# Kernel optimization log

Hardware: AMD Instinct MI355X
Metric: run time of the kernel (lower is better)

The kernel has to match this reference:

```python
import jax, jax.numpy as jnp
import numpy as np

N = 200_000   # nodes in batched graph
E = 400_000   # edges
D = 128       # embed_dim
L = 5         # num_layer
G = 1000      # number of graphs in batch
ATOM_V = 119  # atom vocab (OGB)
BOND_V = 5    # bond vocab (OGB)
OUT = 128     # output_dim
EPS = 1e-5


def setup_inputs() -> dict:
    key = jax.random.key(0)
    ks = jax.random.split(key, 16)
    inp = {
        "nfeat": jax.random.randint(ks[0], (N,), 0, ATOM_V),
        "efeat": jax.random.randint(ks[1], (E,), 0, BOND_V),
        "src": jax.random.randint(ks[2], (E,), 0, N),
        "dst": jax.random.randint(ks[3], (E,), 0, N),
        "node2graph": jnp.sort(jax.random.randint(ks[4], (N,), 0, G)),
        # learned parameters
        "atom_emb": jax.random.normal(ks[5], (ATOM_V, D), jnp.float32) * 0.02,
        "edge_emb": jax.random.normal(ks[6], (L, BOND_V, D), jnp.float32) * 0.02,
        "W": jax.random.normal(ks[7], (L, D, D), jnp.float32) * 0.02,
        "b": jnp.zeros((L, D), jnp.float32),
        "gamma": jnp.ones((L, D), jnp.float32),
        "beta": jnp.zeros((L, D), jnp.float32),
        "W1": jax.random.normal(ks[8], (D, D), jnp.float32) * 0.02,
        "b1": jnp.zeros((D,), jnp.float32),
        "W2": jax.random.normal(ks[9], (D, OUT), jnp.float32) * 0.02,
        "b2": jnp.zeros((OUT,), jnp.float32),
    }
    return inp


def reference(nfeat, efeat, src, dst, node2graph,
              atom_emb, edge_emb, W, b, gamma, beta, W1, b1, W2, b2):
    h = atom_emb[nfeat]                                  # [N, D]
    # in-degree + 1 (GCNConvLayer degree norm)
    deg = jax.ops.segment_sum(jnp.ones((E,), h.dtype), dst, num_segments=N) + 1.0
    for l in range(L):
        e = edge_emb[l][efeat]                           # [E, D] edge encoder
        m = h[src] + e                                   # u_add_e
        neigh = jax.ops.segment_sum(m, dst, num_segments=N)  # fn.sum -> 'neigh'
        h = ((h + neigh) / deg[:, None]) @ W[l] + b[l]   # project_node_feat
        # batch norm over nodes (training-mode batch stats), affine
        mu = jnp.mean(h, axis=0)
        var = jnp.var(h, axis=0)
        h = (h - mu) * jax.lax.rsqrt(var + EPS) * gamma[l] + beta[l]
        h = jax.nn.relu(h)                               # activation; dropout=eval
    # global mean pooling per graph
    cnt = jax.ops.segment_sum(jnp.ones((N,), h.dtype), node2graph, num_segments=G)
    g = jax.ops.segment_sum(h, node2graph, num_segments=G) / jnp.maximum(cnt, 1.0)[:, None]
    # predict MLP (dropout in eval mode = identity)
    out = jax.nn.relu(g @ W1 + b1) @ W2 + b2             # [G, OUT]
    return out
```

## Files before the change

kernel.cpp:

```cpp
#include <hip/hip_runtime.h>
#include <hip/hip_bf16.h>
#include <cstddef>

#define NN 200000
#define NE 400000
#define DD 128
#define NL 5
#define NG 1000
#define BOND_V 5
#define BM 32
#define NBLK (NN / BM)
#define MAXD 16
#define CHUNK 200
#define NB_SCAN 200
#define CH 1000
#define SB 125
#define EPS 1e-5f
#define XS 136

typedef __bf16 bf16x8 __attribute__((ext_vector_type(8)));
typedef float floatx4 __attribute__((ext_vector_type(4)));

__device__ __forceinline__ unsigned short f2bf(float f) {
    unsigned int u = __float_as_uint(f);
    u = (u + 0x7fffu + ((u >> 16) & 1u)) >> 16;
    return (unsigned short)u;
}
__device__ __forceinline__ float bf2f(unsigned short s) {
    return __uint_as_float(((unsigned int)s) << 16);
}
__device__ __forceinline__ float4 bf4_to_f4(uint2 v) {
    float4 o;
    o.x = __uint_as_float(v.x << 16);
    o.y = __uint_as_float(v.x & 0xffff0000u);
    o.z = __uint_as_float(v.y << 16);
    o.w = __uint_as_float(v.y & 0xffff0000u);
    return o;
}
__device__ __forceinline__ float4 actv4(float4 h, float4 sc, float4 sh) {
    float4 o;
    o.x = fmaxf(0.f, h.x * sc.x + sh.x);
    o.y = fmaxf(0.f, h.y * sc.y + sh.y);
    o.z = fmaxf(0.f, h.z * sc.z + sh.z);
    o.w = fmaxf(0.f, h.w * sc.w + sh.w);
    return o;
}

__global__ void k_setup1(const int* __restrict__ dst, int* __restrict__ cnt,
                         const int* __restrict__ n2g, float* __restrict__ gcnt,
                         const float* __restrict__ W, unsigned short* __restrict__ Wht,
                         unsigned short* __restrict__ Wlt) {
    int e = blockIdx.x * blockDim.x + threadIdx.x;
    if (e < NE) atomicAdd(&cnt[dst[e]], 1);
    if (e < NN) atomicAdd(&gcnt[n2g[e]], 1.0f);
    if (e < NL * DD * DD) {
        int l = e / (DD * DD), rem = e % (DD * DD);
        int k = rem / DD, n = rem % DD;
        float v = W[e];
        unsigned short hb = f2bf(v);
        unsigned short lb = f2bf(v - bf2f(hb));
        size_t o = (size_t)l * DD * DD + (size_t)n * DD + k;
        Wht[o] = hb; Wlt[o] = lb;
    }
}

__global__ void k_scan1(const int* __restrict__ cnt, int* __restrict__ bsum) {
    __shared__ int sh[256];
    int b = blockIdx.x, t = threadIdx.x;
    int s = 0;
    if (t < CH / 4) {
        int base = b * CH + t * 4;
        s = cnt[base] + cnt[base + 1] + cnt[base + 2] + cnt[base + 3];
    }
    sh[t] = s;
    __syncthreads();
    if (t == 0) {
        int tot = 0;
        for (int i = 0; i < CH / 4; i++) tot += sh[i];
        bsum[b] = tot;
    }
}

__global__ void k_scan2(const int* __restrict__ bsum, int* __restrict__ bpre,
                        int* __restrict__ off) {
    if (threadIdx.x == 0) {
        int run = 0;
        for (int i = 0; i < NB_SCAN; i++) { bpre[i] = run; run += bsum[i]; }
        off[NN] = NE;
    }
}

__global__ void k_scan3(const int* __restrict__ cnt, const int* __restrict__ bpre,
                        int* __restrict__ off, int* __restrict__ cur,
                        float* __restrict__ rdeg) {
    __shared__ int sh[256];
    int b = blockIdx.x, t = threadIdx.x;
    int base = b * CH + t * 4;
    int c0 = 0, c1 = 0, c2 = 0, c3 = 0, s = 0;
    if (t < CH / 4) {
        c0 = cnt[base]; c1 = cnt[base + 1]; c2 = cnt[base + 2]; c3 = cnt[base + 3];
        s = c0 + c1 + c2 + c3;
    }
    sh[t] = s;
    __syncthreads();
    if (t == 0) {
        int run = bpre[b];
        for (int i = 0; i < CH / 4; i++) { int v = sh[i]; sh[i] = run; run += v; }
    }
    __syncthreads();
    if (t < CH / 4) {
        int run = sh[t];
        off[base] = run; cur[base] = run; run += c0;
        off[base + 1] = run; cur[base + 1] = run; run += c1;
        off[base + 2] = run; cur[base + 2] = run; run += c2;
        off[base + 3] = run; cur[base + 3] = run;
        rdeg[base]     = 1.0f / (float)(c0 + 1);
        rdeg[base + 1] = 1.0f / (float)(c1 + 1);
        rdeg[base + 2] = 1.0f / (float)(c2 + 1);
        rdeg[base + 3] = 1.0f / (float)(c3 + 1);
    }
}

__global__ void k_bucket(const int* __restrict__ src, const int* __restrict__ dst,
                         const int* __restrict__ efeat, int* __restrict__ cur,
                         int* __restrict__ esrc, int* __restrict__ eft) {
    int e = blockIdx.x * blockDim.x + threadIdx.x;
    if (e < NE) {
        int p = atomicAdd(&cur[dst[e]], 1);
        esrc[p] = src[e];
        eft[p] = efeat[e];
    }
}

__global__ void k_pad(const int* __restrict__ off, const int* __restrict__ esrc,
                      const int* __restrict__ eft, const int* __restrict__ nfeat,
                      int* __restrict__ pent, int* __restrict__ pent0,
                      int* __restrict__ bperm, int* __restrict__ gmax) {
    __shared__ int offL[BM + 1];
    __shared__ int degS[BM];
    __shared__ int sortIdx[BM];
    __shared__ int gmaxS[8];
    int b = blockIdx.x, tid = threadIdx.x;
    if (tid <= BM) offL[tid] = off[b * BM + tid];
    __syncthreads();
    if (tid < BM) degS[tid] = offL[tid + 1] - offL[tid];
    __syncthreads();
    if (tid < BM) {
        int d = degS[tid], rank = 0;
        #pragma unroll
        for (int j = 0; j < BM; j++)
            rank += (degS[j] > d) || (degS[j] == d && j < tid);
        sortIdx[rank] = tid;
    }
    __syncthreads();
    if (tid < 8) {
        int g = degS[sortIdx[tid * 4]];
        gmaxS[tid] = g;
        gmax[b * 8 + tid] = g;
    }
    if (tid < BM) bperm[b * BM + tid] = sortIdx[tid];
    __syncthreads();
    for (int idx = tid; idx < BM * MAXD; idx += 256) {
        int p = idx & 31, j = idx >> 5, g = p >> 2;
        int gm = gmaxS[g]; if (gm > MAXD) gm = MAXD;
        if (j < gm) {
            int row = sortIdx[p];
            int d = degS[row];
            int v, v0;
            if (j < d) {
                int e = offL[row] + j;
                int s = esrc[e], f = eft[e];
                v = s | (f << 18);
                v0 = nfeat[s] | (f << 18);
            } else { v = (5 << 18); v0 = (5 << 18); }
            pent[(size_t)b * MAXD * BM + j * BM + p] = v;
            pent0[(size_t)b * MAXD * BM + j * BM + p] = v0;
        }
    }
}

__global__ __launch_bounds__(256, 4)
void k_fused(const void* __restrict__ basep, const int* __restrict__ nfeat, int first,
             const int* __restrict__ off, const int* __restrict__ esrc,
             const int* __restrict__ eft, const int* __restrict__ pentsel,
             const int* __restrict__ bperm, const int* __restrict__ gmax,
             const float* __restrict__ eemb, const float* __restrict__ rdeg,
             const float* __restrict__ scP, const float* __restrict__ shP,
             const unsigned short* __restrict__ Wht, const unsigned short* __restrict__ Wlt,
             const float* __restrict__ bias,
             unsigned short* __restrict__ C, float* __restrict__ part) {
    __shared__ unsigned short Xh[BM * XS];
    __shared__ unsigned short Xl[BM * XS];
    __shared__ float eSr[6 * DD];
    __shared__ int pentL[BM * MAXD];
    __shared__ int offL[BM + 1];
    __shared__ int permL[BM];
    __shared__ int gmL[8];

    const float* baseF = (const float*)basep;
    const unsigned short* baseB = (const unsigned short*)basep;

    int tid = threadIdx.x;
    int n0 = blockIdx.x * BM;
    if (tid < 160) *(float4*)(eSr + tid * 4) = *(const float4*)(eemb + tid * 4);
    else if (tid < 192) *(float4*)(eSr + tid * 4) = (float4){0.f, 0.f, 0.f, 0.f};
    if (tid <= BM) offL[tid] = off[n0 + tid];
    if (tid < BM) permL[tid] = bperm[blockIdx.x * BM + tid];
    if (tid < 8) gmL[tid] = gmax[blockIdx.x * 8 + tid];
    {
        const int2* pg = (const int2*)(pentsel + (size_t)blockIdx.x * MAXD * BM);
        *(int2*)(pentL + tid * 2) = pg[tid];
    }

    int lane32 = tid & 31, grp = tid >> 5;
    int c4 = lane32 << 2;
    float4 sc4, sh4;
    if (!first) {
        sc4 = *(const float4*)(scP + c4);
        sh4 = *(const float4*)(shP + c4);
    }
    __syncthreads();

    int rows[4];
    #pragma unroll
    for (int i = 0; i < 4; i++) rows[i] = permL[grp * 4 + i];

    float4 acc[4];
    #pragma unroll
    for (int i = 0; i < 4; i++) {
        int n = n0 + rows[i];
        if (first) {
            acc[i] = *(const float4*)(baseF + (size_t)nfeat[n] * DD + c4);
        } else {
            uint2 g = *(const uint2*)(baseB + (size_t)n * DD + c4);
            acc[i] = actv4(bf4_to_f4(g), sc4, sh4);
        }
    }

    int gmx = gmL[grp];
    int jmax = gmx < MAXD ? gmx : MAXD;
    const int* pL = pentL + grp * 4;
    int j = 0;
    if (first) {
        for (; j + 2 <= jmax; j += 2) {
            int a0 = pL[j*32+0], a1 = pL[j*32+1], a2 = pL[j*32+2], a3 = pL[j*32+3];
            int b0 = pL[j*32+32], b1 = pL[j*32+33], b2 = pL[j*32+34], b3 = pL[j*32+35];
            float4 ha0 = *(const float4*)(baseF + (size_t)(a0 & 0x3FFFF) * DD + c4);
            float4 ha1 = *(const float4*)(baseF + (size_t)(a1 & 0x3FFFF) * DD + c4);
            float4 ha2 = *(const float4*)(baseF + (size_t)(a2 & 0x3FFFF) * DD + c4);
            float4 ha3 = *(const float4*)(baseF + (size_t)(a3 & 0x3FFFF) * DD + c4);
            float4 hb0 = *(const float4*)(baseF + (size_t)(b0 & 0x3FFFF) * DD + c4);
            float4 hb1 = *(const float4*)(baseF + (size_t)(b1 & 0x3FFFF) * DD + c4);
            float4 hb2 = *(const float4*)(baseF + (size_t)(b2 & 0x3FFFF) * DD + c4);
            float4 hb3 = *(const float4*)(baseF + (size_t)(b3 & 0x3FFFF) * DD + c4);
            int fa0 = a0 >> 18, fa1 = a1 >> 18, fa2 = a2 >> 18, fa3 = a3 >> 18;
            int fb0 = b0 >> 18, fb1 = b1 >> 18, fb2 = b2 >> 18, fb3 = b3 >> 18;
            float wa0 = (fa0 == 5) ? 0.f : 1.f, wa1 = (fa1 == 5) ? 0.f : 1.f;
            float wa2 = (fa2 == 5) ? 0.f : 1.f, wa3 = (fa3 == 5) ? 0.f : 1.f;
            float wb0 = (fb0 == 5) ? 0.f : 1.f, wb1 = (fb1 == 5) ? 0.f : 1.f;
            float wb2 = (fb2 == 5) ? 0.f : 1.f, wb3 = (fb3 == 5) ? 0.f : 1.f;
            float4 ea0 = *(const float4*)(eSr + fa0 * DD + c4);
            float4 ea1 = *(const float4*)(eSr + fa1 * DD + c4);
            float4 ea2 = *(const float4*)(eSr + fa2 * DD + c4);
            float4 ea3 = *(const float4*)(eSr + fa3 * DD + c4);
            float4 eb0 = *(const float4*)(eSr + fb0 * DD + c4);
            float4 eb1 = *(const float4*)(eSr + fb1 * DD + c4);
            float4 eb2 = *(const float4*)(eSr + fb2 * DD + c4);
            float4 eb3 = *(const float4*)(eSr + fb3 * DD + c4);
            acc[0].x += (ha0.x + ea0.x) * wa0 + (hb0.x + eb0.x) * wb0;
            acc[0].y += (ha0.y + ea0.y) * wa0 + (hb0.y + eb0.y) * wb0;
            acc[0].z += (ha0.z + ea0.z) * wa0 + (hb0.z + eb0.z) * wb0;
            acc[0].w += (ha0.w + ea0.w) * wa0 + (hb0.w + eb0.w) * wb0;
            acc[1].x += (ha1.x + ea1.x) * wa1 + (hb1.x + eb1.x) * wb1;
            acc[1].y += (ha1.y + ea1.y) * wa1 + (hb1.y + eb1.y) * wb1;
            acc[1].z += (ha1.z + ea1.z) * wa1 + (hb1.z + eb1.z) * wb1;
            acc[1].w += (ha1.w + ea1.w) * wa1 + (hb1.w + eb1.w) * wb1;
            acc[2].x += (ha2.x + ea2.x) * wa2 + (hb2.x + eb2.x) * wb2;
            acc[2].y += (ha2.y + ea2.y) * wa2 + (hb2.y + eb2.y) * wb2;
            acc[2].z += (ha2.z + ea2.z) * wa2 + (hb2.z + eb2.z) * wb2;
            acc[2].w += (ha2.w + ea2.w) * wa2 + (hb2.w + eb2.w) * wb2;
            acc[3].x += (ha3.x + ea3.x) * wa3 + (hb3.x + eb3.x) * wb3;
            acc[3].y += (ha3.y + ea3.y) * wa3 + (hb3.y + eb3.y) * wb3;
            acc[3].z += (ha3.z + ea3.z) * wa3 + (hb3.z + eb3.z) * wb3;
            acc[3].w += (ha3.w + ea3.w) * wa3 + (hb3.w + eb3.w) * wb3;
        }
        for (; j < jmax; j++) {
            int a0 = pL[j*32+0], a1 = pL[j*32+1], a2 = pL[j*32+2], a3 = pL[j*32+3];
            float4 h0 = *(const float4*)(baseF + (size_t)(a0 & 0x3FFFF) * DD + c4);
            float4 h1 = *(const float4*)(baseF + (size_t)(a1 & 0x3FFFF) * DD + c4);
            float4 h2 = *(const float4*)(baseF + (size_t)(a2 & 0x3FFFF) * DD + c4);
            float4 h3 = *(const float4*)(baseF + (size_t)(a3 & 0x3FFFF) * DD + c4);
            int f0 = a0 >> 18, f1 = a1 >> 18, f2 = a2 >> 18, f3 = a3 >> 18;
            float w0 = (f0 == 5) ? 0.f : 1.f, w1 = (f1 == 5) ? 0.f : 1.f;
            float w2 = (f2 == 5) ? 0.f : 1.f, w3 = (f3 == 5) ? 0.f : 1.f;
            float4 e0 = *(const float4*)(eSr + f0 * DD + c4);
            float4 e1 = *(const float4*)(eSr + f1 * DD + c4);
            float4 e2 = *(const float4*)(eSr + f2 * DD + c4);
            float4 e3 = *(const float4*)(eSr + f3 * DD + c4);
            acc[0].x += (h0.x + e0.x) * w0; acc[0].y += (h0.y + e0.y) * w0;
            acc[0].z += (h0.z + e0.z) * w0; acc[0].w += (h0.w + e0.w) * w0;
            acc[1].x += (h1.x + e1.x) * w1; acc[1].y += (h1.y + e1.y) * w1;
            acc[1].z += (h1.z + e1.z) * w1; acc[1].w += (h1.w + e1.w) * w1;
            acc[2].x += (h2.x + e2.x) * w2; acc[2].y += (h2.y + e2.y) * w2;
            acc[2].z += (h2.z + e2.z) * w2; acc[2].w += (h2.w + e2.w) * w2;
            acc[3].x += (h3.x + e3.x) * w3; acc[3].y += (h3.y + e3.y) * w3;
            acc[3].z += (h3.z + e3.z) * w3; acc[3].w += (h3.w + e3.w) * w3;
        }
    } else {
        for (; j + 2 <= jmax; j += 2) {
            int a0 = pL[j*32+0], a1 = pL[j*32+1], a2 = pL[j*32+2], a3 = pL[j*32+3];
            int b0 = pL[j*32+32], b1 = pL[j*32+33], b2 = pL[j*32+34], b3 = pL[j*32+35];
            uint2 ga0 = *(const uint2*)(baseB + (size_t)(a0 & 0x3FFFF) * DD + c4);
            uint2 ga1 = *(const uint2*)(baseB + (size_t)(a1 & 0x3FFFF) * DD + c4);
            uint2 ga2 = *(const uint2*)(baseB + (size_t)(a2 & 0x3FFFF) * DD + c4);
            uint2 ga3 = *(const uint2*)(baseB + (size_t)(a3 & 0x3FFFF) * DD + c4);
            uint2 gb0 = *(const uint2*)(baseB + (size_t)(b0 & 0x3FFFF) * DD + c4);
            uint2 gb1 = *(const uint2*)(baseB + (size_t)(b1 & 0x3FFFF) * DD + c4);
            uint2 gb2 = *(const uint2*)(baseB + (size_t)(b2 & 0x3FFFF) * DD + c4);
            uint2 gb3 = *(const uint2*)(baseB + (size_t)(b3 & 0x3FFFF) * DD + c4);
            float4 ha0 = actv4(bf4_to_f4(ga0), sc4, sh4);
            float4 ha1 = actv4(bf4_to_f4(ga1), sc4, sh4);
            float4 ha2 = actv4(bf4_to_f4(ga2), sc4, sh4);
            float4 ha3 = actv4(bf4_to_f4(ga3), sc4, sh4);
            float4 hb0 = actv4(bf4_to_f4(gb0), sc4, sh4);
            float4 hb1 = actv4(bf4_to_f4(gb1), sc4, sh4);
            float4 hb2 = actv4(bf4_to_f4(gb2), sc4, sh4);
            float4 hb3 = actv4(bf4_to_f4(gb3), sc4, sh4);
            int fa0 = a0 >> 18, fa1 = a1 >> 18, fa2 = a2 >> 18, fa3 = a3 >> 18;
            int fb0 = b0 >> 18, fb1 = b1 >> 18, fb2 = b2 >> 18, fb3 = b3 >> 18;
            float wa0 = (fa0 == 5) ? 0.f : 1.f, wa1 = (fa1 == 5) ? 0.f : 1.f;
            float wa2 = (fa2 == 5) ? 0.f : 1.f, wa3 = (fa3 == 5) ? 0.f : 1.f;
            float wb0 = (fb0 == 5) ? 0.f : 1.f, wb1 = (fb1 == 5) ? 0.f : 1.f;
            float wb2 = (fb2 == 5) ? 0.f : 1.f, wb3 = (fb3 == 5) ? 0.f : 1.f;
            float4 ea0 = *(const float4*)(eSr + fa0 * DD + c4);
            float4 ea1 = *(const float4*)(eSr + fa1 * DD + c4);
            float4 ea2 = *(const float4*)(eSr + fa2 * DD + c4);
            float4 ea3 = *(const float4*)(eSr + fa3 * DD + c4);
            float4 eb0 = *(const float4*)(eSr + fb0 * DD + c4);
            float4 eb1 = *(const float4*)(eSr + fb1 * DD + c4);
            float4 eb2 = *(const float4*)(eSr + fb2 * DD + c4);
            float4 eb3 = *(const float4*)(eSr + fb3 * DD + c4);
            acc[0].x += (ha0.x + ea0.x) * wa0 + (hb0.x + eb0.x) * wb0;
            acc[0].y += (ha0.y + ea0.y) * wa0 + (hb0.y + eb0.y) * wb0;
            acc[0].z += (ha0.z + ea0.z) * wa0 + (hb0.z + eb0.z) * wb0;
            acc[0].w += (ha0.w + ea0.w) * wa0 + (hb0.w + eb0.w) * wb0;
            acc[1].x += (ha1.x + ea1.x) * wa1 + (hb1.x + eb1.x) * wb1;
            acc[1].y += (ha1.y + ea1.y) * wa1 + (hb1.y + eb1.y) * wb1;
            acc[1].z += (ha1.z + ea1.z) * wa1 + (hb1.z + eb1.z) * wb1;
            acc[1].w += (ha1.w + ea1.w) * wa1 + (hb1.w + eb1.w) * wb1;
            acc[2].x += (ha2.x + ea2.x) * wa2 + (hb2.x + eb2.x) * wb2;
            acc[2].y += (ha2.y + ea2.y) * wa2 + (hb2.y + eb2.y) * wb2;
            acc[2].z += (ha2.z + ea2.z) * wa2 + (hb2.z + eb2.z) * wb2;
            acc[2].w += (ha2.w + ea2.w) * wa2 + (hb2.w + eb2.w) * wb2;
            acc[3].x += (ha3.x + ea3.x) * wa3 + (hb3.x + eb3.x) * wb3;
            acc[3].y += (ha3.y + ea3.y) * wa3 + (hb3.y + eb3.y) * wb3;
            acc[3].z += (ha3.z + ea3.z) * wa3 + (hb3.z + eb3.z) * wb3;
            acc[3].w += (ha3.w + ea3.w) * wa3 + (hb3.w + eb3.w) * wb3;
        }
        for (; j < jmax; j++) {
            int a0 = pL[j*32+0], a1 = pL[j*32+1], a2 = pL[j*32+2], a3 = pL[j*32+3];
            uint2 g0 = *(const uint2*)(baseB + (size_t)(a0 & 0x3FFFF) * DD + c4);
            uint2 g1 = *(const uint2*)(baseB + (size_t)(a1 & 0x3FFFF) * DD + c4);
            uint2 g2 = *(const uint2*)(baseB + (size_t)(a2 & 0x3FFFF) * DD + c4);
            uint2 g3 = *(const uint2*)(baseB + (size_t)(a3 & 0x3FFFF) * DD + c4);
            float4 h0 = actv4(bf4_to_f4(g0), sc4, sh4);
            float4 h1 = actv4(bf4_to_f4(g1), sc4, sh4);
            float4 h2 = actv4(bf4_to_f4(g2), sc4, sh4);
            float4 h3 = actv4(bf4_to_f4(g3), sc4, sh4);
            int f0 = a0 >> 18, f1 = a1 >> 18, f2 = a2 >> 18, f3 = a3 >> 18;
            float w0 = (f0 == 5) ? 0.f : 1.f, w1 = (f1 == 5) ? 0.f : 1.f;
            float w2 = (f2 == 5) ? 0.f : 1.f, w3 = (f3 == 5) ? 0.f : 1.f;
            float4 e0 = *(const float4*)(eSr + f0 * DD + c4);
            float4 e1 = *(const float4*)(eSr + f1 * DD + c4);
            float4 e2 = *(const float4*)(eSr + f2 * DD + c4);
            float4 e3 = *(const float4*)(eSr + f3 * DD + c4);
            acc[0].x += (h0.x + e0.x) * w0; acc[0].y += (h0.y + e0.y) * w0;
            acc[0].z += (h0.z + e0.z) * w0; acc[0].w += (h0.w + e0.w) * w0;
            acc[1].x += (h1.x + e1.x) * w1; acc[1].y += (h1.y + e1.y) * w1;
            acc[1].z += (h1.z + e1.z) * w1; acc[1].w += (h1.w + e1.w) * w1;
            acc[2].x += (h2.x + e2.x) * w2; acc[2].y += (h2.y + e2.y) * w2;
            acc[2].z += (h2.z + e2.z) * w2; acc[2].w += (h2.w + e2.w) * w2;
            acc[3].x += (h3.x + e3.x) * w3; acc[3].y += (h3.y + e3.y) * w3;
            acc[3].z += (h3.z + e3.z) * w3; acc[3].w += (h3.w + e3.w) * w3;
        }
    }

    if (gmx > MAXD) {
        #pragma unroll
        for (int i = 0; i < 4; i++) {
            int row = rows[i];
            for (int e = offL[row] + MAXD; e < offL[row + 1]; e++) {
                int s = esrc[e], f = eft[e];
                float4 hv;
                if (first) {
                    hv = *(const float4*)(baseF + (size_t)nfeat[s] * DD + c4);
                } else {
                    uint2 g = *(const uint2*)(baseB + (size_t)s * DD + c4);
                    hv = actv4(bf4_to_f4(g), sc4, sh4);
                }
                const float* ep = eSr + f * DD + c4;
                acc[i].x += hv.x + ep[0]; acc[i].y += hv.y + ep[1];
                acc[i].z += hv.z + ep[2]; acc[i].w += hv.w + ep[3];
            }
        }
    }

    #pragma unroll
    for (int i = 0; i < 4; i++) {
        int r = rows[i];
        float rd = rdeg[n0 + r];
        float ax = acc[i].x * rd, ay = acc[i].y * rd, az = acc[i].z * rd, aw = acc[i].w * rd;
        unsigned short h0 = f2bf(ax), h1 = f2bf(ay), h2 = f2bf(az), h3 = f2bf(aw);
        unsigned short l0 = f2bf(ax - bf2f(h0));
        unsigned short l1 = f2bf(ay - bf2f(h1));
        unsigned short l2 = f2bf(az - bf2f(h2));
        unsigned short l3 = f2bf(aw - bf2f(h3));
        uint2 hv2, lv2;
        hv2.x = (unsigned)h0 | ((unsigned)h1 << 16);
        hv2.y = (unsigned)h2 | ((unsigned)h3 << 16);
        lv2.x = (unsigned)l0 | ((unsigned)l1 << 16);
        lv2.y = (unsigned)l2 | ((unsigned)l3 << 16);
        *(uint2*)(Xh + r * XS + c4) = hv2;
        *(uint2*)(Xl + r * XS + c4) = lv2;
    }
    __syncthreads();

    int lane = tid & 63, w = tid >> 6;
    int m16 = lane & 15, quad = lane >> 4;
    int rowTile = w & 1;
    int colBase = (w >> 1) << 6;
    int rowA = rowTile * 16 + m16;

    floatx4 acc4[4];
    #pragma unroll
    for (int t = 0; t < 4; t++) acc4[t] = (floatx4){0.f, 0.f, 0.f, 0.f};

    #pragma unroll
    for (int kp = 0; kp < 4; kp++) {
        bf16x8 ah = *(const bf16x8*)(Xh + rowA * XS + kp * 32 + quad * 8);
        bf16x8 al = *(const bf16x8*)(Xl + rowA * XS + kp * 32 + quad * 8);
        #pragma unroll
        for (int t = 0; t < 4; t++) {
            int ncol = colBase + t * 16 + m16;
            bf16x8 bh = *(const bf16x8*)(Wht + (size_t)ncol * DD + kp * 32 + quad * 8);
            bf16x8 bl = *(const bf16x8*)(Wlt + (size_t)ncol * DD + kp * 32 + quad * 8);
            acc4[t] = __builtin_amdgcn_mfma_f32_16x16x32_bf16(ah, bh, acc4[t], 0, 0, 0);
            acc4[t] = __builtin_amdgcn_mfma_f32_16x16x32_bf16(ah, bl, acc4[t], 0, 0, 0);
            acc4[t] = __builtin_amdgcn_mfma_f32_16x16x32_bf16(al, bh, acc4[t], 0, 0, 0);
        }
    }
    __syncthreads();

    float* redS = eSr;
    float* redQ = eSr + 2 * DD;
    unsigned short* Cs = Xh;
    #pragma unroll
    for (int t = 0; t < 4; t++) {
        int col = colBase + t * 16 + m16;
        float bv = bias[col];
        float s = 0.f, q = 0.f;
        #pragma unroll
        for (int rr = 0; rr < 4; rr++) {
            float vv = acc4[t][rr] + bv;
            s += vv; q += vv * vv;
            Cs[(rowTile * 16 + quad * 4 + rr) * XS + col] = f2bf(vv);
        }
        s += __shfl_xor(s, 16); q += __shfl_xor(q, 16);
        s += __shfl_xor(s, 32); q += __shfl_xor(q, 32);
        if (lane < 16) { redS[rowTile * DD + col] = s; redQ[rowTile * DD + col] = q; }
    }
    __syncthreads();

    #pragma unroll
    for (int it = 0; it < 2; it++) {
        int idx = it * 256 + tid;
        int row = idx >> 4, q16 = idx & 15;
        uint4 v = *(const uint4*)(Cs + row * XS + q16 * 8);
        *(uint4*)(C + (size_t)(n0 + row) * DD + q16 * 8) = v;
    }
    if (tid < DD) {
        float ss = redS[tid] + redS[DD + tid];
        float qq = redQ[tid] + redQ[DD + tid];
        part[(size_t)blockIdx.x * 256 + tid] = ss;
        part[(size_t)blockIdx.x * 256 + DD + tid] = qq;
    }
}

__global__ void k_stats(const float* __restrict__ part, float* __restrict__ acc,
                        int* __restrict__ cnt,
                        const float* __restrict__ gamma, const float* __restrict__ beta,
                        float* __restrict__ scale, float* __restrict__ shift) {
    int t = threadIdx.x;
    float s = 0.f;
    int base = blockIdx.x * (NBLK / SB);
    for (int i = 0; i < NBLK / SB; i++)
        s += part[(size_t)(base + i) * 256 + t];
    atomicAdd(&acc[t], s);
    __threadfence();
    __shared__ int lastS;
    __syncthreads();
    if (t == 0) lastS = (atomicAdd(cnt, 1) == SB - 1);
    __syncthreads();
    if (lastS && t < DD) {
        float Sv = atomicAdd(&acc[t], 0.0f);
        float Qv = atomicAdd(&acc[DD + t], 0.0f);
        float m = Sv / (float)NN;
        float v = Qv / (float)NN - m * m;
        float rs = rsqrtf(v + EPS);
        float sc = rs * gamma[t];
        scale[t] = sc;
        shift[t] = beta[t] - m * sc;
    }
}

__global__ void k_bnpool(const unsigned short* __restrict__ A, const int* __restrict__ n2g,
                         const float* __restrict__ scale, const float* __restrict__ shift,
                         float* __restrict__ gsum) {
    int j = threadIdx.x;
    int n0 = blockIdx.x * CHUNK;
    float sc = scale[j], sh = shift[j];
    int cur = n2g[n0];
    float acc = 0.f;
    for (int i = 0; i < CHUNK; i++) {
        int n = n0 + i;
        int gg = n2g[n];
        if (gg != cur) {
            atomicAdd(&gsum[(size_t)cur * DD + j], acc);
            acc = 0.f;
            cur = gg;
        }
        float x = bf2f(A[(size_t)n * DD + j]);
        acc += fmaxf(0.f, x * sc + sh);
    }
    atomicAdd(&gsum[(size_t)cur * DD + j], acc);
}

__global__ void k_mlp(const float* __restrict__ gsum, const float* __restrict__ gcnt,
                      const float* __restrict__ W1, const float* __restrict__ b1,
                      const float* __restrict__ W2, const float* __restrict__ b2,
                      float* __restrict__ out) {
    __shared__ float gs[DD], hs[DD];
    int gid = blockIdx.x, j = threadIdx.x;
    float inv = 1.0f / fmaxf(gcnt[gid], 1.0f);
    gs[j] = gsum[(size_t)gid * DD + j] * inv;
    __syncthreads();
    float a = b1[j];
    for (int k = 0; k < DD; k++) a += gs[k] * W1[k * DD + j];
    hs[j] = fmaxf(a, 0.f);
    __syncthreads();
    float o = b2[j];
    for (int k = 0; k < DD; k++) o += hs[k] * W2[k * DD + j];
    out[(size_t)gid * DD + j] = o;
}

extern "C" void kernel_launch(void* const* d_in, const int* in_sizes, int n_in,
                              void* d_out, int out_size, void* d_ws, size_t ws_size,
                              hipStream_t stream) {
    const int*   nfeat = (const int*)d_in[0];
    const int*   efeat = (const int*)d_in[1];
    const int*   src   = (const int*)d_in[2];
    const int*   dst   = (const int*)d_in[3];
    const int*   n2g   = (const int*)d_in[4];
    const float* aemb  = (const float*)d_in[5];
    const float* eemb  = (const float*)d_in[6];
    const float* Wl    = (const float*)d_in[7];
    const float* bl    = (const float*)d_in[8];
    const float* gam   = (const float*)d_in[9];
    const float* bet   = (const float*)d_in[10];
    const float* W1    = (const float*)d_in[11];
    const float* b1    = (const float*)d_in[12];
    const float* W2    = (const float*)d_in[13];
    const float* b2    = (const float*)d_in[14];
    float* out = (float*)d_out;

    unsigned short* H0 = (unsigned short*)d_ws;
    unsigned short* H1 = H0 + (size_t)NN * DD;
    float* rdeg   = (float*)(H1 + (size_t)NN * DD);
    float* gsum   = rdeg + NN;
    float* gcnt   = gsum + (size_t)NG * DD;
    float* scaleA = gcnt + NG;
    float* shiftA = scaleA + NL * DD;
    float* accS   = shiftA + NL * DD;
    int*   scnt   = (int*)(accS + NL * 256);
    float* part   = (float*)(scnt + 16);
    unsigned short* Wht = (unsigned short*)(part + (size_t)NBLK * 256);
    unsigned short* Wlt = Wht + (size_t)NL * DD * DD;
    int* off   = (int*)(Wlt + (size_t)NL * DD * DD);
    int* cur   = off + NN + 1;
    int* esrc  = cur + NN;
    int* eft   = esrc + NE;
    int* cnt   = eft + NE;
    int* bsum  = cnt + NN;
    int* bpre  = bsum + NB_SCAN;
    int* bperm = bpre + NB_SCAN;
    int* gmax  = bperm + (size_t)NBLK * BM;
    int* pent  = gmax + (size_t)NBLK * 8;
    int* pent0 = pent + (size_t)NBLK * MAXD * BM;

    hipMemsetAsync(gsum, 0, (size_t)(NG * DD + NG) * sizeof(float), stream);
    hipMemsetAsync(accS, 0, (size_t)(NL * 256) * sizeof(float) + 16 * sizeof(int), stream);
    hipMemsetAsync(cnt, 0, (size_t)NN * sizeof(int), stream);

    k_setup1<<<(NE + 255) / 256, 256, 0, stream>>>(dst, cnt, n2g, gcnt, Wl, Wht, Wlt);
    k_scan1<<<NB_SCAN, 256, 0, stream>>>(cnt, bsum);
    k_scan2<<<1, 64, 0, stream>>>(bsum, bpre, off);
    k_scan3<<<NB_SCAN, 256, 0, stream>>>(cnt, bpre, off, cur, rdeg);
    k_bucket<<<(NE + 255) / 256, 256, 0, stream>>>(src, dst, efeat, cur, esrc, eft);
    k_pad<<<NBLK, 256, 0, stream>>>(off, esrc, eft, nfeat, pent, pent0, bperm, gmax);

    unsigned short* hcur = H0;
    for (int l = 0; l < NL; l++) {
        const void* base = (l == 0) ? (const void*)aemb : (const void*)hcur;
        unsigned short* hnext = (l == 0) ? H0 : ((hcur == H0) ? H1 : H0);
        const int* psel = (l == 0) ? pent0 : pent;
        const float* scP = scaleA + (size_t)((l == 0) ? 0 : (l - 1)) * DD;
        const float* shP = shiftA + (size_t)((l == 0) ? 0 : (l - 1)) * DD;
        k_fused<<<NBLK, 256, 0, stream>>>(base, nfeat, (l == 0) ? 1 : 0,
                                          off, esrc, eft, psel, bperm, gmax,
                                          eemb + (size_t)l * BOND_V * DD, rdeg,
                                          scP, shP,
                                          Wht + (size_t)l * DD * DD,
                                          Wlt + (size_t)l * DD * DD,
                                          bl + (size_t)l * DD, hnext, part);
        k_stats<<<SB, 256, 0, stream>>>(part, accS + l * 256, scnt + l,
                                        gam + (size_t)l * DD, bet + (size_t)l * DD,
                                        scaleA + (size_t)l * DD, shiftA + (size_t)l * DD);
        hcur = hnext;
    }
    k_bnpool<<<NN / CHUNK, DD, 0, stream>>>(hcur, n2g,
                                            scaleA + (size_t)(NL - 1) * DD,
                                            shiftA + (size_t)(NL - 1) * DD, gsum);
    k_mlp<<<NG, DD, 0, stream>>>(gsum, gcnt, W1, b1, W2, b2, out);
}
```

Before: 1.071 ms.

## Fuse batch-norm statistics reduction into fused layer kernel via sharded atomics

Removes the separate k_stats kernel and partial-sum buffer. Each fused-layer block now atomically adds its per-channel sum and sum of squares into one of 16 shards, and the last block to finish (found with a counter) reduces the shards and writes the BN scale and shift. This saves a kernel launch and a partial-buffer round trip per layer, at the cost of global atomic contention and a serialized tail in the last block. The pooling CHUNK is also halved to give that kernel more blocks.

```diff
diff --git a/kernel.cpp b/kernel.cpp
--- a/kernel.cpp
+++ b/kernel.cpp
@@ -11,10 +11,10 @@
 #define BM 32
 #define NBLK (NN / BM)
 #define MAXD 16
-#define CHUNK 200
+#define CHUNK 100
 #define NB_SCAN 200
 #define CH 1000
-#define SB 125
+#define NSH 16
 #define EPS 1e-5f
 #define XS 136
 
@@ -188,7 +188,10 @@
              const float* __restrict__ scP, const float* __restrict__ shP,
              const unsigned short* __restrict__ Wht, const unsigned short* __restrict__ Wlt,
              const float* __restrict__ bias,
-             unsigned short* __restrict__ C, float* __restrict__ part) {
+             unsigned short* __restrict__ C,
+             float* __restrict__ musum, int* __restrict__ cntL,
+             const float* __restrict__ gamC, const float* __restrict__ betC,
+             float* __restrict__ scO, float* __restrict__ shO) {
     __shared__ unsigned short Xh[BM * XS];
     __shared__ unsigned short Xl[BM * XS];
     __shared__ float eSr[6 * DD];
@@ -196,6 +199,7 @@
     __shared__ int offL[BM + 1];
     __shared__ int permL[BM];
     __shared__ int gmL[8];
+    __shared__ int lastF;
 
     const float* baseF = (const float*)basep;
     const unsigned short* baseB = (const unsigned short*)basep;
@@ -478,38 +482,34 @@
         uint4 v = *(const uint4*)(Cs + row * XS + q16 * 8);
         *(uint4*)(C + (size_t)(n0 + row) * DD + q16 * 8) = v;
     }
+
+    int shard = blockIdx.x & (NSH - 1);
     if (tid < DD) {
         float ss = redS[tid] + redS[DD + tid];
         float qq = redQ[tid] + redQ[DD + tid];
-        part[(size_t)blockIdx.x * 256 + tid] = ss;
-        part[(size_t)blockIdx.x * 256 + DD + tid] = qq;
-    }
-}
-
-__global__ void k_stats(const float* __restrict__ part, float* __restrict__ acc,
-                        int* __restrict__ cnt,
-                        const float* __restrict__ gamma, const float* __restrict__ beta,
-                        float* __restrict__ scale, float* __restrict__ shift) {
-    int t = threadIdx.x;
-    float s = 0.f;
-    int base = blockIdx.x * (NBLK / SB);
-    for (int i = 0; i < NBLK / SB; i++)
-        s += part[(size_t)(base + i) * 256 + t];
-    atomicAdd(&acc[t], s);
+        atomicAdd(&musum[(size_t)tid * NSH + shard], ss);
+        atomicAdd(&musum[(size_t)(DD + tid) * NSH + shard], qq);
+    }
     __threadfence();
-    __shared__ int lastS;
-    __syncthreads();
-    if (t == 0) lastS = (atomicAdd(cnt, 1) == SB - 1);
-    __syncthreads();
-    if (lastS && t < DD) {
-        float Sv = atomicAdd(&acc[t], 0.0f);
-        float Qv = atomicAdd(&acc[DD + t], 0.0f);
-        float m = Sv / (float)NN;
-        float v = Qv / (float)NN - m * m;
-        float rs = rsqrtf(v + EPS);
-        float sc = rs * gamma[t];
-        scale[t] = sc;
-        shift[t] = beta[t] - m * sc;
+    __syncthreads();
+    if (tid == 0) lastF = (atomicAdd(cntL, 1) == NBLK - 1);
+    __syncthreads();
+    if (lastF) {
+        float s = 0.f;
+        #pragma unroll
+        for (int i = 0; i < NSH; i++)
+            s += atomicAdd(&musum[(size_t)tid * NSH + i], 0.0f);
+        eSr[tid] = s;
+        __syncthreads();
+        if (tid < DD) {
+            float Sv = eSr[tid], Qv = eSr[DD + tid];
+            float m = Sv / (float)NN;
+            float v = Qv / (float)NN - m * m;
+            float rs = rsqrtf(v + EPS);
+            float sc = rs * gamC[tid];
+            scO[tid] = sc;
+            shO[tid] = betC[tid] - m * sc;
+        }
     }
 }
 
@@ -581,9 +581,8 @@
     float* scaleA = gcnt + NG;
     float* shiftA = scaleA + NL * DD;
     float* accS   = shiftA + NL * DD;
-    int*   scnt   = (int*)(accS + NL * 256);
-    float* part   = (float*)(scnt + 16);
-    unsigned short* Wht = (unsigned short*)(part + (size_t)NBLK * 256);
+    int*   scnt   = (int*)(accS + (size_t)NL * 256 * NSH);
+    unsigned short* Wht = (unsigned short*)(scnt + 16);
     unsigned short* Wlt = Wht + (size_t)NL * DD * DD;
     int* off   = (int*)(Wlt + (size_t)NL * DD * DD);
     int* cur   = off + NN + 1;
@@ -598,7 +597,7 @@
     int* pent0 = pent + (size_t)NBLK * MAXD * BM;
 
     hipMemsetAsync(gsum, 0, (size_t)(NG * DD + NG) * sizeof(float), stream);
-    hipMemsetAsync(accS, 0, (size_t)(NL * 256) * sizeof(float) + 16 * sizeof(int), stream);
+    hipMemsetAsync(accS, 0, (size_t)(NL * 256 * NSH) * sizeof(float) + 16 * sizeof(int), stream);
     hipMemsetAsync(cnt, 0, (size_t)NN * sizeof(int), stream);
 
     k_setup1<<<(NE + 255) / 256, 256, 0, stream>>>(dst, cnt, n2g, gcnt, Wl, Wht, Wlt);
@@ -621,10 +620,10 @@
                                           scP, shP,
                                           Wht + (size_t)l * DD * DD,
                                           Wlt + (size_t)l * DD * DD,
-                                          bl + (size_t)l * DD, hnext, part);
-        k_stats<<<SB, 256, 0, stream>>>(part, accS + l * 256, scnt + l,
-                                        gam + (size_t)l * DD, bet + (size_t)l * DD,
-                                        scaleA + (size_t)l * DD, shiftA + (size_t)l * DD);
+                                          bl + (size_t)l * DD, hnext,
+                                          accS + (size_t)l * 256 * NSH, scnt + l,
+                                          gam + (size_t)l * DD, bet + (size_t)l * DD,
+                                          scaleA + (size_t)l * DD, shiftA + (size_t)l * DD);
         hcur = hnext;
     }
     k_bnpool<<<NN / CHUNK, DD, 0, stream>>>(hcur, n2g,
```

Result: slower. 3.925 ms (+266.6%).
